# Performance work log

Measured on AMD Instinct MI355X. Metric: run time of the kernel, lower is better.

Reference implementation:

```python
import jax, jax.numpy as jnp
import numpy as np

Q, M, D = 4096, 100000, 1536

def _l2norm(x, eps=1e-12):
    return x / jnp.maximum(jnp.linalg.norm(x, axis=1, keepdims=True), eps)

def setup_inputs() -> dict:
    key = jax.random.key(0)
    kq, km = jax.random.split(key)
    # patch features are L2-normalized in _extract_patches (F.normalize p=2)
    query = _l2norm(jax.random.normal(kq, (Q, D), dtype=jnp.float32))
    memory = _l2norm(jax.random.normal(km, (M, D), dtype=jnp.float32))
    return {"query": query, "memory": memory}

def reference(query, memory):
    # torch.cdist(query, memory) (p=2) followed by min over memory dim.
    # dist^2 = |q|^2 + |m|^2 - 2 q.m  -> sqrt, clamped at 0 for numerics.
    q2 = jnp.sum(query * query, axis=1, keepdims=True)          # [Q, 1]
    m2 = jnp.sum(memory * memory, axis=1)                        # [M]
    d2 = q2 + m2[None, :] - 2.0 * (query @ memory.T)             # [Q, M]
    dists = jnp.sqrt(jnp.maximum(d2, 0.0))
    nn_dists = jnp.min(dists, axis=1)                            # [Q]
    anomaly_score = jnp.max(nn_dists)                            # scalar, predict()'s score
    return nn_dists, anomaly_score
```

## Files before the change

### kernel.cpp

```cpp
#include <hip/hip_runtime.h>
#include <hip/hip_bf16.h>
#include <float.h>


#define QN 4096
#define MN 100000
#define MP 100096
#define DN 1536
#define BK 32
#define NKIT (DN / BK)

typedef __attribute__((ext_vector_type(8))) short short8;
typedef __attribute__((ext_vector_type(4))) float float4v;
typedef __attribute__((ext_vector_type(4))) short short4v;
typedef __attribute__((address_space(1))) const unsigned g_u32;
typedef __attribute__((address_space(3))) unsigned l_u32;

__device__ __forceinline__ short f2bf(float f) {
    unsigned u = __float_as_uint(f);
    u += 0x7FFFu + ((u >> 16) & 1u);
    return (short)(u >> 16);
}
__device__ __forceinline__ unsigned encf(float f) {
    unsigned u = __float_as_uint(f);
    return (u & 0x80000000u) ? ~u : (u | 0x80000000u);
}
__device__ __forceinline__ float decf(unsigned e) {
    unsigned u = (e & 0x80000000u) ? (e & 0x7FFFFFFFu) : ~e;
    return __uint_as_float(u);
}
__device__ __forceinline__ void gload_lds16(const void* g, void* l) {
    __builtin_amdgcn_global_load_lds((g_u32*)g, (l_u32*)l, 16, 0, 0);
}

__global__ void init_min(unsigned* __restrict__ dminEnc) {
    int i = blockIdx.x * blockDim.x + threadIdx.x;
    if (i < QN) dminEnc[i] = 0xFF7FFFFFu;
}

__global__ void cvt_bf16(const float* __restrict__ src, short* __restrict__ dst,
                         long n_valid, long n_total) {
    long i = ((long)blockIdx.x * blockDim.x + threadIdx.x) * 4;
    if (i >= n_total) return;
    if (i + 4 <= n_valid) {
        float4 v = *(const float4*)(src + i);
        short4v o = { f2bf(v.x), f2bf(v.y), f2bf(v.z), f2bf(v.w) };
        *(short4v*)(dst + i) = o;
    } else {
        for (int j = 0; j < 4; ++j)
            if (i + j < n_total) dst[i + j] = (i + j < n_valid) ? f2bf(src[i + j]) : 0;
    }
}

__global__ __launch_bounds__(256)
void nn_gemm_bf16(const short* __restrict__ qB, const short* __restrict__ mB,
                  unsigned* __restrict__ dminEnc)
{
    __shared__ __align__(16) short As[128 * BK];
    __shared__ __align__(16) short Bs[128 * BK];
    __shared__ unsigned qmin[128];

    const int tid  = threadIdx.x;
    const int lane = tid & 63;
    const int wave = tid >> 6;
    const int wrow = wave >> 1;
    const int wcol = wave & 1;
    const int quad = lane >> 4;
    const int l16  = lane & 15;

    const int qb = blockIdx.x * 128;
    const int mb = blockIdx.y * 128;

    if (tid < 128) qmin[tid] = 0xFFFFFFFFu;

    const int srow = wave * 32 + (lane >> 2);
    const int scol = (lane & 3) * 8;
    const short* gA0 = qB + (size_t)(qb + srow) * DN + scol;
    const short* gA1 = gA0 + (size_t)16 * DN;
    const short* gB0 = mB + (size_t)(mb + srow) * DN + scol;
    const short* gB1 = gB0 + (size_t)16 * DN;
    short* lA0 = As + (wave * 32) * BK;
    short* lA1 = As + (wave * 32 + 16) * BK;
    short* lB0 = Bs + (wave * 32) * BK;
    short* lB1 = Bs + (wave * 32 + 16) * BK;

    float4v acc[4][4];
#pragma unroll
    for (int mi = 0; mi < 4; ++mi)
#pragma unroll
        for (int ni = 0; ni < 4; ++ni)
            acc[mi][ni] = (float4v){0.f, 0.f, 0.f, 0.f};

    for (int kk = 0; kk < NKIT; ++kk) {
        const size_t ko = (size_t)kk * BK;
        gload_lds16(gA0 + ko, lA0);
        gload_lds16(gA1 + ko, lA1);
        gload_lds16(gB0 + ko, lB0);
        gload_lds16(gB1 + ko, lB1);
        __syncthreads();

        short8 af[4], bf[4];
#pragma unroll
        for (int mi = 0; mi < 4; ++mi)
            af[mi] = *(const short8*)&As[(wrow * 64 + mi * 16 + l16) * BK + quad * 8];
#pragma unroll
        for (int ni = 0; ni < 4; ++ni)
            bf[ni] = *(const short8*)&Bs[(wcol * 64 + ni * 16 + l16) * BK + quad * 8];

#pragma unroll
        for (int mi = 0; mi < 4; ++mi)
#pragma unroll
            for (int ni = 0; ni < 4; ++ni)
                acc[mi][ni] = __builtin_amdgcn_mfma_f32_16x16x32_bf16(
                    af[mi], bf[ni], acc[mi][ni], 0, 0, 0);
        __syncthreads();
    }

#pragma unroll
    for (int mi = 0; mi < 4; ++mi) {
#pragma unroll
        for (int r = 0; r < 4; ++r) {
            float v = FLT_MAX;
#pragma unroll
            for (int ni = 0; ni < 4; ++ni) {
                int gcol = mb + wcol * 64 + ni * 16 + l16;
                float d2 = fmaf(-2.0f, acc[mi][ni][r], 2.0f);
                v = fminf(v, (gcol < MN) ? d2 : FLT_MAX);
            }
            v = fminf(v, __shfl_xor(v, 1));
            v = fminf(v, __shfl_xor(v, 2));
            v = fminf(v, __shfl_xor(v, 4));
            v = fminf(v, __shfl_xor(v, 8));
            if (l16 == 0) {
                int rloc = wrow * 64 + mi * 16 + quad * 4 + r;
                atomicMin(&qmin[rloc], encf(v));
            }
        }
    }
    __syncthreads();
    if (tid < 128) atomicMin(&dminEnc[qb + tid], qmin[tid]);
}

#define LDSS 40
__global__ __launch_bounds__(256, 2)
void nn_gemm_f32(const float* __restrict__ query, const float* __restrict__ memory,
                 unsigned* __restrict__ dminEnc)
{
    __shared__ __align__(16) short As[128 * LDSS];
    __shared__ __align__(16) short Bs[128 * LDSS];
    __shared__ unsigned qmin[128];

    const int tid = threadIdx.x, lane = tid & 63, wave = tid >> 6;
    const int wrow = wave >> 1, wcol = wave & 1, quad = lane >> 4, l16 = lane & 15;
    const int qb = blockIdx.x * 128, mb = blockIdx.y * 128;
    if (tid < 128) qmin[tid] = 0xFFFFFFFFu;

    int rowS[4], c4S[4];
    const float *aPtr[4], *bPtr[4];
    bool bValid[4];
#pragma unroll
    for (int s = 0; s < 4; ++s) {
        int idx = s * 256 + tid, row = idx >> 3, c4 = idx & 7;
        rowS[s] = row; c4S[s] = c4;
        aPtr[s] = query + (size_t)(qb + row) * DN + c4 * 4;
        int gr = mb + row;
        bValid[s] = (gr < MN);
        bPtr[s] = memory + (size_t)(bValid[s] ? gr : 0) * DN + c4 * 4;
    }
    float4 aReg[4], bReg[4];
#pragma unroll
    for (int s = 0; s < 4; ++s) {
        aReg[s] = *(const float4*)(aPtr[s]);
        bReg[s] = bValid[s] ? *(const float4*)(bPtr[s]) : make_float4(0.f, 0.f, 0.f, 0.f);
    }
    float4v acc[4][4];
#pragma unroll
    for (int mi = 0; mi < 4; ++mi)
#pragma unroll
        for (int ni = 0; ni < 4; ++ni) acc[mi][ni] = (float4v){0.f, 0.f, 0.f, 0.f};

    for (int kk = 0; kk < NKIT; ++kk) {
#pragma unroll
        for (int s = 0; s < 4; ++s) {
            short4v pa = { f2bf(aReg[s].x), f2bf(aReg[s].y), f2bf(aReg[s].z), f2bf(aReg[s].w) };
            short4v pb = { f2bf(bReg[s].x), f2bf(bReg[s].y), f2bf(bReg[s].z), f2bf(bReg[s].w) };
            *(short4v*)&As[rowS[s] * LDSS + c4S[s] * 4] = pa;
            *(short4v*)&Bs[rowS[s] * LDSS + c4S[s] * 4] = pb;
        }
        __syncthreads();
        if (kk + 1 < NKIT) {
            const int ko = (kk + 1) * BK;
#pragma unroll
            for (int s = 0; s < 4; ++s) {
                aReg[s] = *(const float4*)(aPtr[s] + ko);
                bReg[s] = bValid[s] ? *(const float4*)(bPtr[s] + ko)
                                    : make_float4(0.f, 0.f, 0.f, 0.f);
            }
        }
        short8 af[4], bf[4];
#pragma unroll
        for (int mi = 0; mi < 4; ++mi)
            af[mi] = *(const short8*)&As[(wrow * 64 + mi * 16 + l16) * LDSS + quad * 8];
#pragma unroll
        for (int ni = 0; ni < 4; ++ni)
            bf[ni] = *(const short8*)&Bs[(wcol * 64 + ni * 16 + l16) * LDSS + quad * 8];
#pragma unroll
        for (int mi = 0; mi < 4; ++mi)
#pragma unroll
            for (int ni = 0; ni < 4; ++ni)
                acc[mi][ni] = __builtin_amdgcn_mfma_f32_16x16x32_bf16(
                    af[mi], bf[ni], acc[mi][ni], 0, 0, 0);
        __syncthreads();
    }
#pragma unroll
    for (int mi = 0; mi < 4; ++mi) {
#pragma unroll
        for (int r = 0; r < 4; ++r) {
            float v = FLT_MAX;
#pragma unroll
            for (int ni = 0; ni < 4; ++ni) {
                int gcol = mb + wcol * 64 + ni * 16 + l16;
                float d2 = fmaf(-2.0f, acc[mi][ni][r], 2.0f);
                v = fminf(v, (gcol < MN) ? d2 : FLT_MAX);
            }
            v = fminf(v, __shfl_xor(v, 1));
            v = fminf(v, __shfl_xor(v, 2));
            v = fminf(v, __shfl_xor(v, 4));
            v = fminf(v, __shfl_xor(v, 8));
            if (l16 == 0)
                atomicMin(&qmin[wrow * 64 + mi * 16 + quad * 4 + r], encf(v));
        }
    }
    __syncthreads();
    if (tid < 128) atomicMin(&dminEnc[qb + tid], qmin[tid]);
}

__global__ void finalize(const unsigned* __restrict__ dminEnc, float* __restrict__ out) {
    __shared__ float red[256];
    const int tid = threadIdx.x;
    float mx = 0.f;
    for (int i = tid; i < QN; i += 256) {
        float d2 = decf(dminEnc[i]);
        float d = sqrtf(fmaxf(d2, 0.f));
        out[i] = d;
        mx = fmaxf(mx, d);
    }
    red[tid] = mx;
    __syncthreads();
    for (int s = 128; s > 0; s >>= 1) {
        if (tid < s) red[tid] = fmaxf(red[tid], red[tid + s]);
        __syncthreads();
    }
    if (tid == 0) out[QN] = red[0];
}

extern "C" void kernel_launch(void* const* d_in, const int* in_sizes, int n_in,
                              void* d_out, int out_size, void* d_ws, size_t ws_size,
                              hipStream_t stream)
{
    const float* query  = (const float*)d_in[0];
    const float* memory = (const float*)d_in[1];
    float* out = (float*)d_out;

    const size_t memB_elems = (size_t)MP * DN;
    const size_t qB_elems   = (size_t)QN * DN;
    const size_t need = memB_elems * 2 + qB_elems * 2 + (size_t)QN * 4;

    if (ws_size >= need) {
        short* mB = (short*)d_ws;
        short* qB = mB + memB_elems;
        unsigned* dminEnc = (unsigned*)(qB + qB_elems);

        hipLaunchKernelGGL(init_min, dim3((QN + 255) / 256), dim3(256), 0, stream, dminEnc);
        {
            long nv = (long)MN * DN, nt = (long)memB_elems;
            int blocks = (int)((nt / 4 + 255) / 256);
            hipLaunchKernelGGL(cvt_bf16, dim3(blocks), dim3(256), 0, stream,
                               memory, mB, nv, nt);
        }
        {
            long nv = (long)qB_elems, nt = (long)qB_elems;
            int blocks = (int)((nt / 4 + 255) / 256);
            hipLaunchKernelGGL(cvt_bf16, dim3(blocks), dim3(256), 0, stream,
                               query, qB, nv, nt);
        }
        hipLaunchKernelGGL(nn_gemm_bf16, dim3(QN / 128, MP / 128), dim3(256), 0, stream,
                           qB, mB, dminEnc);
        hipLaunchKernelGGL(finalize, dim3(1), dim3(256), 0, stream, dminEnc, out);
    } else {
        unsigned* dminEnc = (unsigned*)d_ws;
        hipLaunchKernelGGL(init_min, dim3((QN + 255) / 256), dim3(256), 0, stream, dminEnc);
        hipLaunchKernelGGL(nn_gemm_f32, dim3(QN / 128, (MN + 127) / 128), dim3(256), 0, stream,
                           query, memory, dminEnc);
        hipLaunchKernelGGL(finalize, dim3(1), dim3(256), 0, stream, dminEnc, out);
    }
}
```

Baseline: 2.246 ms.

## Switch nearest-neighbour GEMM from bf16 to scaled fp8 32x32x64 MFMA

Inputs are now quantized to fp8 with a scale of 64 instead of bf16, and the inner product runs on the scaled fp8 32x32x64 MFMA instruction, with block scales undoing the 64x factor. The K tile grows to 64 bytes with an XOR-swizzled LDS layout to avoid bank conflicts, and the epilogue reduction is remapped to the 32x32 output layout. This halves conversion and GEMM memory traffic and uses the higher-throughput fp8 matrix path. The cost is much coarser precision on distances (fp8 e4m3 on unit-norm 1536-d vectors), which risks failing tolerance.

Result: slower. 2.865 ms (+27.6%).

```diff
diff --git a/kernel.cpp b/kernel.cpp
--- a/kernel.cpp
+++ b/kernel.cpp
@@ -7,12 +7,16 @@
 #define MN 100000
 #define MP 100096
 #define DN 1536
-#define BK 32
-#define NKIT (DN / BK)
-
-typedef __attribute__((ext_vector_type(8))) short short8;
-typedef __attribute__((ext_vector_type(4))) float float4v;
-typedef __attribute__((ext_vector_type(4))) short short4v;
+#define BKF 64
+#define NKF (DN / BKF)
+#define SCALE_M6 0x79797979
+
+typedef __attribute__((ext_vector_type(8)))  int   int8v;
+typedef __attribute__((ext_vector_type(4)))  int   int4v;
+typedef __attribute__((ext_vector_type(16))) float float16v;
+typedef __attribute__((ext_vector_type(8)))  short short8;
+typedef __attribute__((ext_vector_type(4)))  short short4v;
+typedef __attribute__((ext_vector_type(4)))  float float4v;
 typedef __attribute__((address_space(1))) const unsigned g_u32;
 typedef __attribute__((address_space(3))) unsigned l_u32;
 
@@ -38,26 +42,35 @@
     if (i < QN) dminEnc[i] = 0xFF7FFFFFu;
 }
 
-__global__ void cvt_bf16(const float* __restrict__ src, short* __restrict__ dst,
-                         long n_valid, long n_total) {
-    long i = ((long)blockIdx.x * blockDim.x + threadIdx.x) * 4;
+__global__ void cvt_fp8(const float* __restrict__ src, unsigned char* __restrict__ dst,
+                        long n_valid, long n_total) {
+    long i = ((long)blockIdx.x * blockDim.x + threadIdx.x) * 8;
     if (i >= n_total) return;
-    if (i + 4 <= n_valid) {
-        float4 v = *(const float4*)(src + i);
-        short4v o = { f2bf(v.x), f2bf(v.y), f2bf(v.z), f2bf(v.w) };
-        *(short4v*)(dst + i) = o;
+    if (i + 8 <= n_valid) {
+        float4 v0 = *(const float4*)(src + i);
+        float4 v1 = *(const float4*)(src + i + 4);
+        int p0 = __builtin_amdgcn_cvt_pk_fp8_f32(v0.x * 64.f, v0.y * 64.f, 0, 0);
+        p0     = __builtin_amdgcn_cvt_pk_fp8_f32(v0.z * 64.f, v0.w * 64.f, p0, 1);
+        int p1 = __builtin_amdgcn_cvt_pk_fp8_f32(v1.x * 64.f, v1.y * 64.f, 0, 0);
+        p1     = __builtin_amdgcn_cvt_pk_fp8_f32(v1.z * 64.f, v1.w * 64.f, p1, 1);
+        int2 o = { p0, p1 };
+        *(int2*)(dst + i) = o;
     } else {
-        for (int j = 0; j < 4; ++j)
-            if (i + j < n_total) dst[i + j] = (i + j < n_valid) ? f2bf(src[i + j]) : 0;
+        for (int j = 0; j < 8; ++j)
+            if (i + j < n_total) {
+                float f = (i + j < n_valid) ? src[i + j] * 64.f : 0.f;
+                int p = __builtin_amdgcn_cvt_pk_fp8_f32(f, 0.f, 0, 0);
+                dst[i + j] = (unsigned char)(p & 0xFF);
+            }
     }
 }
 
 __global__ __launch_bounds__(256)
-void nn_gemm_bf16(const short* __restrict__ qB, const short* __restrict__ mB,
-                  unsigned* __restrict__ dminEnc)
+void nn_gemm_fp8(const unsigned char* __restrict__ qF, const unsigned char* __restrict__ mF,
+                 unsigned* __restrict__ dminEnc)
 {
-    __shared__ __align__(16) short As[128 * BK];
-    __shared__ __align__(16) short Bs[128 * BK];
+    __shared__ __align__(16) unsigned char As[128 * BKF];
+    __shared__ __align__(16) unsigned char Bs[128 * BKF];
     __shared__ unsigned qmin[128];
 
     const int tid  = threadIdx.x;
@@ -65,8 +78,6 @@
     const int wave = tid >> 6;
     const int wrow = wave >> 1;
     const int wcol = wave & 1;
-    const int quad = lane >> 4;
-    const int l16  = lane & 15;
 
     const int qb = blockIdx.x * 128;
     const int mb = blockIdx.y * 128;
@@ -74,56 +85,75 @@
     if (tid < 128) qmin[tid] = 0xFFFFFFFFu;
 
     const int srow = wave * 32 + (lane >> 2);
-    const int scol = (lane & 3) * 8;
-    const short* gA0 = qB + (size_t)(qb + srow) * DN + scol;
-    const short* gA1 = gA0 + (size_t)16 * DN;
-    const short* gB0 = mB + (size_t)(mb + srow) * DN + scol;
-    const short* gB1 = gB0 + (size_t)16 * DN;
-    short* lA0 = As + (wave * 32) * BK;
-    short* lA1 = As + (wave * 32 + 16) * BK;
-    short* lB0 = Bs + (wave * 32) * BK;
-    short* lB1 = Bs + (wave * 32 + 16) * BK;
-
-    float4v acc[4][4];
-#pragma unroll
-    for (int mi = 0; mi < 4; ++mi)
-#pragma unroll
-        for (int ni = 0; ni < 4; ++ni)
-            acc[mi][ni] = (float4v){0.f, 0.f, 0.f, 0.f};
-
-    for (int kk = 0; kk < NKIT; ++kk) {
-        const size_t ko = (size_t)kk * BK;
+    const int jb   = (((lane & 3) ^ ((lane >> 3) & 3))) * 16;
+    const unsigned char* gA0 = qF + (size_t)(qb + srow) * DN + jb;
+    const unsigned char* gA1 = gA0 + (size_t)16 * DN;
+    const unsigned char* gB0 = mF + (size_t)(mb + srow) * DN + jb;
+    const unsigned char* gB1 = gB0 + (size_t)16 * DN;
+    unsigned char* lA0 = As + (wave * 32) * BKF;
+    unsigned char* lA1 = As + (wave * 32 + 16) * BKF;
+    unsigned char* lB0 = Bs + (wave * 32) * BKF;
+    unsigned char* lB1 = Bs + (wave * 32 + 16) * BKF;
+
+    const int r31 = lane & 31;
+    const int sw  = (r31 >> 1) & 3;
+    const int c0  = (lane >> 5) * 2;
+    const int po0 = (c0 ^ sw) * 16;
+    const int po1 = ((c0 + 1) ^ sw) * 16;
+
+    float16v acc[2][2];
+#pragma unroll
+    for (int mi = 0; mi < 2; ++mi)
+#pragma unroll
+        for (int ni = 0; ni < 2; ++ni)
+#pragma unroll
+            for (int e = 0; e < 16; ++e) acc[mi][ni][e] = 0.f;
+
+    for (int kk = 0; kk < NKF; ++kk) {
+        const size_t ko = (size_t)kk * BKF;
         gload_lds16(gA0 + ko, lA0);
         gload_lds16(gA1 + ko, lA1);
         gload_lds16(gB0 + ko, lB0);
         gload_lds16(gB1 + ko, lB1);
         __syncthreads();
 
-        short8 af[4], bf[4];
-#pragma unroll
-        for (int mi = 0; mi < 4; ++mi)
-            af[mi] = *(const short8*)&As[(wrow * 64 + mi * 16 + l16) * BK + quad * 8];
-#pragma unroll
-        for (int ni = 0; ni < 4; ++ni)
-            bf[ni] = *(const short8*)&Bs[(wcol * 64 + ni * 16 + l16) * BK + quad * 8];
-
-#pragma unroll
-        for (int mi = 0; mi < 4; ++mi)
-#pragma unroll
-            for (int ni = 0; ni < 4; ++ni)
-                acc[mi][ni] = __builtin_amdgcn_mfma_f32_16x16x32_bf16(
-                    af[mi], bf[ni], acc[mi][ni], 0, 0, 0);
-        __syncthreads();
-    }
-
-#pragma unroll
-    for (int mi = 0; mi < 4; ++mi) {
-#pragma unroll
-        for (int r = 0; r < 4; ++r) {
+        int8v af[2], bf[2];
+#pragma unroll
+        for (int mi = 0; mi < 2; ++mi) {
+            const int rb = (wrow * 64 + mi * 32 + r31) * BKF;
+            int4v lo = *(const int4v*)&As[rb + po0];
+            int4v hi = *(const int4v*)&As[rb + po1];
+            af[mi][0] = lo[0]; af[mi][1] = lo[1]; af[mi][2] = lo[2]; af[mi][3] = lo[3];
+            af[mi][4] = hi[0]; af[mi][5] = hi[1]; af[mi][6] = hi[2]; af[mi][7] = hi[3];
+        }
+#pragma unroll
+        for (int ni = 0; ni < 2; ++ni) {
+            const int rb = (wcol * 64 + ni * 32 + r31) * BKF;
+            int4v lo = *(const int4v*)&Bs[rb + po0];
+            int4v hi = *(const int4v*)&Bs[rb + po1];
+            bf[ni][0] = lo[0]; bf[ni][1] = lo[1]; bf[ni][2] = lo[2]; bf[ni][3] = lo[3];
+            bf[ni][4] = hi[0]; bf[ni][5] = hi[1]; bf[ni][6] = hi[2]; bf[ni][7] = hi[3];
+        }
+
+#pragma unroll
+        for (int mi = 0; mi < 2; ++mi)
+#pragma unroll
+            for (int ni = 0; ni < 2; ++ni)
+                acc[mi][ni] = __builtin_amdgcn_mfma_scale_f32_32x32x64_f8f6f4(
+                    af[mi], bf[ni], acc[mi][ni],
+                    0 , 0 ,
+                    0, SCALE_M6, 0, SCALE_M6);
+        __syncthreads();
+    }
+
+#pragma unroll
+    for (int mi = 0; mi < 2; ++mi) {
+#pragma unroll
+        for (int r = 0; r < 16; ++r) {
             float v = FLT_MAX;
 #pragma unroll
-            for (int ni = 0; ni < 4; ++ni) {
-                int gcol = mb + wcol * 64 + ni * 16 + l16;
+            for (int ni = 0; ni < 2; ++ni) {
+                int gcol = mb + wcol * 64 + ni * 32 + r31;
                 float d2 = fmaf(-2.0f, acc[mi][ni][r], 2.0f);
                 v = fminf(v, (gcol < MN) ? d2 : FLT_MAX);
             }
@@ -131,8 +161,9 @@
             v = fminf(v, __shfl_xor(v, 2));
             v = fminf(v, __shfl_xor(v, 4));
             v = fminf(v, __shfl_xor(v, 8));
-            if (l16 == 0) {
-                int rloc = wrow * 64 + mi * 16 + quad * 4 + r;
+            v = fminf(v, __shfl_xor(v, 16));
+            if (r31 == 0) {
+                int rloc = wrow * 64 + mi * 32 + (r & 3) + 8 * (r >> 2) + 4 * (lane >> 5);
                 atomicMin(&qmin[rloc], encf(v));
             }
         }
@@ -141,6 +172,8 @@
     if (tid < 128) atomicMin(&dminEnc[qb + tid], qmin[tid]);
 }
 
+#define BK 32
+#define NKIT (DN / BK)
 #define LDSS 40
 __global__ __launch_bounds__(256, 2)
 void nn_gemm_f32(const float* __restrict__ query, const float* __restrict__ memory,
@@ -262,30 +295,28 @@
     const float* memory = (const float*)d_in[1];
     float* out = (float*)d_out;
 
-    const size_t memB_elems = (size_t)MP * DN;
-    const size_t qB_elems   = (size_t)QN * DN;
-    const size_t need = memB_elems * 2 + qB_elems * 2 + (size_t)QN * 4;
+    const size_t memF_bytes = (size_t)MP * DN;
+    const size_t qF_bytes   = (size_t)QN * DN;
+    const size_t need = memF_bytes + qF_bytes + (size_t)QN * 4;
 
     if (ws_size >= need) {
-        short* mB = (short*)d_ws;
-        short* qB = mB + memB_elems;
-        unsigned* dminEnc = (unsigned*)(qB + qB_elems);
+        unsigned char* mF = (unsigned char*)d_ws;
+        unsigned char* qF = mF + memF_bytes;
+        unsigned* dminEnc = (unsigned*)(qF + qF_bytes);
 
         hipLaunchKernelGGL(init_min, dim3((QN + 255) / 256), dim3(256), 0, stream, dminEnc);
         {
-            long nv = (long)MN * DN, nt = (long)memB_elems;
-            int blocks = (int)((nt / 4 + 255) / 256);
-            hipLaunchKernelGGL(cvt_bf16, dim3(blocks), dim3(256), 0, stream,
-                               memory, mB, nv, nt);
+            long nv = (long)MN * DN, nt = (long)memF_bytes;
+            int blocks = (int)((nt / 8 + 255) / 256);
+            hipLaunchKernelGGL(cvt_fp8, dim3(blocks), dim3(256), 0, stream, memory, mF, nv, nt);
         }
         {
-            long nv = (long)qB_elems, nt = (long)qB_elems;
-            int blocks = (int)((nt / 4 + 255) / 256);
-            hipLaunchKernelGGL(cvt_bf16, dim3(blocks), dim3(256), 0, stream,
-                               query, qB, nv, nt);
-        }
-        hipLaunchKernelGGL(nn_gemm_bf16, dim3(QN / 128, MP / 128), dim3(256), 0, stream,
-                           qB, mB, dminEnc);
+            long nv = (long)qF_bytes, nt = (long)qF_bytes;
+            int blocks = (int)((nt / 8 + 255) / 256);
+            hipLaunchKernelGGL(cvt_fp8, dim3(blocks), dim3(256), 0, stream, query, qF, nv, nt);
+        }
+        hipLaunchKernelGGL(nn_gemm_fp8, dim3(QN / 128, MP / 128), dim3(256), 0, stream,
+                           qF, mF, dminEnc);
         hipLaunchKernelGGL(finalize, dim3(1), dim3(256), 0, stream, dminEnc, out);
     } else {
         unsigned* dminEnc = (unsigned*)d_ws;
```
